# Performance work log

Measured on AMD Instinct MI355X. Metric: run time of the kernel, lower is better.

Reference implementation:

```python
import jax, jax.numpy as jnp
import numpy as np

B, C_IN, N = 2048, 128, 128
M = N - 1  # conv output positions per tree (stride-3 kernel-3 over 3*M gathered triples)


def setup_inputs() -> dict:
    key = jax.random.key(0)
    ks = jax.random.split(key, 8)
    trees = jax.random.normal(ks[0], (B, C_IN, N), jnp.float32)
    trees = trees.at[:, :, 0].set(0.0)  # slot 0 is the zero-pad node
    indexes = jax.random.randint(ks[1], (B, 3 * M), 0, N)

    def wconv(k, o, c):
        return jax.random.normal(k, (o, c, 3), jnp.float32) * 0.05

    return {
        "trees": trees,
        "indexes": indexes,
        "W1": wconv(ks[2], 256, C_IN), "b1": jnp.zeros((256,), jnp.float32),
        "W2": wconv(ks[3], 128, 256), "b2": jnp.zeros((128,), jnp.float32),
        "W3": wconv(ks[4], 64, 128), "b3": jnp.zeros((64,), jnp.float32),
        "W4": jax.random.normal(ks[5], (32, 64), jnp.float32) * 0.1,
        "b4": jnp.zeros((32,), jnp.float32),
        "W5": jax.random.normal(ks[6], (1, 32), jnp.float32) * 0.1,
        "b5": jnp.zeros((1,), jnp.float32),
    }


def _tree_conv(data, idx, W, b):
    # data: [B, C, N]; idx: [B, 3M] of (self, left, right) node indices
    g = jnp.take_along_axis(data, idx[:, None, :], axis=2)        # [B, C, 3M] gather
    g = g.reshape(data.shape[0], data.shape[1], -1, 3)            # [B, C, M, 3]
    out = jnp.einsum('bcmk,ock->bom', g, W) + b[None, :, None]    # Conv1d(k=3, s=3)
    zero = jnp.zeros((out.shape[0], out.shape[1], 1), out.dtype)  # re-prepend zero slot
    return jnp.concatenate([zero, out], axis=2)                   # [B, O, N]


def _tree_layer_norm(data):
    # normalize over (channels, nodes) per tree; torch.std is unbiased (ddof=1)
    mean = jnp.mean(data, axis=(1, 2), keepdims=True)
    std = jnp.std(data, axis=(1, 2), keepdims=True, ddof=1)
    return (data - mean) / (std + 1e-5)


def _leaky(x):
    return jax.nn.leaky_relu(x, 0.01)


def reference(trees, W1, b1, W2, b2, W3, b3, W4, b4, W5, b5, indexes):
    x = _leaky(_tree_layer_norm(_tree_conv(trees, indexes, W1, b1)))
    x = _leaky(_tree_layer_norm(_tree_conv(x, indexes, W2, b2)))
    x = _tree_layer_norm(_tree_conv(x, indexes, W3, b3))
    pooled = jnp.max(x, axis=2)                                   # DynamicPooling -> [B, 64]
    h = _leaky(pooled @ W4.T + b4)
    return h @ W5.T + b5                                          # [B, 1]
```

## Files before the change

kernel.cpp:

```cpp
#include <hip/hip_runtime.h>

typedef unsigned short u16;
typedef __attribute__((ext_vector_type(8)))  short          short8;
typedef __attribute__((ext_vector_type(8)))  unsigned short ushort8v;
typedef __attribute__((ext_vector_type(4)))  unsigned short ushort4v;
typedef __attribute__((ext_vector_type(16))) float          float16v;

__device__ __forceinline__ float bf2f(u16 u){
  union { unsigned int i; float f; } x; x.i = ((unsigned int)u) << 16; return x.f;
}
__device__ __forceinline__ u16 f2bf(float f){
  union { float f; unsigned int i; } x; x.f = f;
  unsigned int u = x.i;
  unsigned int r = (u + 0x7FFFu + ((u >> 16) & 1u)) >> 16;
  return (u16)r;
}
__device__ __forceinline__ float lk(float v){ return v > 0.f ? v : 0.01f*v; }

__global__ void permute_w(const float* __restrict__ W1, const float* __restrict__ W2,
                          const float* __restrict__ W3, u16* __restrict__ ws){
  int t = blockIdx.x*256 + threadIdx.x;
  const float* src; u16* dst; int C, local;
  if (t < 98304)       { src = W1; dst = ws;          C = 128; local = t; }
  else if (t < 196608) { src = W2; dst = ws + 98304;  C = 256; local = t - 98304; }
  else if (t < 221184) { src = W3; dst = ws + 196608; C = 128; local = t - 196608; }
  else return;
  const int NJK  = 3*C/16;
  const int tile = local >> 9, within = local & 511;
  const int lane = within >> 3, e = within & 7;
  const int rb = tile / NJK, jk = tile - rb*NJK;
  const int o  = rb*32 + (lane & 31);
  const int kg = jk*16 + (lane >> 5)*8 + e;
  const int j  = kg / C, c = kg - j*C;
  dst[local] = f2bf(src[o*3*C + c*3 + j]);
}

template<int CIN, int O, int SIN, int OST, int NTL, int NACT, bool LEAKY, bool IS_L3>
__device__ __forceinline__ void do_layer(const u16* __restrict__ Wt,
                                         const float* __restrict__ bias,
                                         const u16* bIn, u16* bOut, float* bOutF,
                                         const int* sidx, float* sstat,
                                         int tid, float* out_mean, float* out_inv)
{
  constexpr int KS  = CIN/16;
  constexpr int NJK = 3*KS;
  static_assert((O/64)*4 == NACT*NTL, "work split mismatch");
  const int w = tid >> 6, lane = tid & 63, l31 = lane & 31, h = lane >> 5;
  const bool active = (w < NACT);
  const int wa = active ? w : 0;

  const int u0  = wa*NTL;
  const int rb  = u0 >> 2;
  const int nt0 = u0 & 3;
  const int r0  = rb * 64;

  const u16* aP[2] = { Wt + ((size_t)(rb*2    )*NJK)*512 + lane*8,
                       Wt + ((size_t)(rb*2 + 1)*NJK)*512 + lane*8 };

  float16v acc[NTL][2];
  float s = 0.f, s2 = 0.f;

  if (active){
    int boff[NTL][3];
#pragma unroll
    for (int n = 0; n < NTL; ++n){
      int m = (nt0 + n)*32 + l31;
#pragma unroll
      for (int j = 0; j < 3; ++j){
        int i = sidx[3*m + j];
        boff[n][j] = i*SIN + h*8;
      }
    }

#pragma unroll
    for (int n = 0; n < NTL; ++n){ acc[n][0] = {}; acc[n][1] = {}; }

#pragma unroll
    for (int jk = 0; jk < NJK; ++jk){
      const int j    = jk / KS;
      const int coff = (jk - j*KS)*16;
      short8 A0 = *(const short8*)(aP[0] + jk*512);
      short8 A1 = *(const short8*)(aP[1] + jk*512);
#pragma unroll
      for (int n = 0; n < NTL; ++n){
        short8 Bf = *(const short8*)(bIn + boff[n][j] + coff);
        acc[n][0] = __builtin_amdgcn_mfma_f32_32x32x16_bf16(A0, Bf, acc[n][0], 0, 0, 0);
        acc[n][1] = __builtin_amdgcn_mfma_f32_32x32x16_bf16(A1, Bf, acc[n][1], 0, 0, 0);
      }
    }

#pragma unroll
    for (int n = 0; n < NTL; ++n){
      const int m = (nt0 + n)*32 + l31;
      const bool valid = (m <= 126);
#pragma unroll
      for (int a = 0; a < 2; ++a)
#pragma unroll
        for (int g = 0; g < 4; ++g){
          const int rowb = r0 + a*32 + 8*g + 4*h;
#pragma unroll
          for (int q = 0; q < 4; ++q){
            float raw = acc[n][a][4*g + q] + bias[rowb + q];
            acc[n][a][4*g + q] = raw;
            if (valid){ s += raw; s2 += raw*raw; }
          }
        }
    }
  }

#pragma unroll
  for (int off = 32; off >= 1; off >>= 1){
    s  += __shfl_down(s,  off, 64);
    s2 += __shfl_down(s2, off, 64);
  }
  if (lane == 0){ sstat[w*2] = s; sstat[w*2+1] = s2; }
  __syncthreads();

  float tot = 0.f, tot2 = 0.f;
#pragma unroll
  for (int q = 0; q < 8; ++q){ tot += sstat[2*q]; tot2 += sstat[2*q+1]; }
  constexpr float CNT = (float)(O * 128);
  const float mean = tot / CNT;
  float var = (tot2 - tot*mean) / (CNT - 1.f);
  var = fmaxf(var, 0.f);
  const float inv = 1.f / (sqrtf(var) + 1e-5f);
  *out_mean = mean; *out_inv = inv;

  if constexpr (!IS_L3){
    if (active){
#pragma unroll
      for (int n = 0; n < NTL; ++n){
        const int m = (nt0 + n)*32 + l31;
        const bool valid = (m <= 126);
#pragma unroll
        for (int a = 0; a < 2; ++a){
#pragma unroll
          for (int g = 0; g < 4; ++g){
            const int rowb = r0 + a*32 + 8*g + 4*h;
            ushort4v pk;
#pragma unroll
            for (int q = 0; q < 4; ++q){
              float f = (acc[n][a][4*g + q] - mean) * inv;
              if constexpr (LEAKY) f = lk(f);
              pk[q] = f2bf(f);
            }
            if (valid) *(ushort4v*)(bOut + (size_t)(m+1)*OST + rowb) = pk;
          }
        }
      }
    }
    if (tid < O/8){
      float f0 = (0.f - mean) * inv;
      if constexpr (LEAKY) f0 = lk(f0);
      const u16 v0 = f2bf(f0);
      ushort8v z;
#pragma unroll
      for (int e = 0; e < 8; ++e) z[e] = v0;
      *(ushort8v*)(bOut + tid*8) = z;
    }
  } else {
    if (active){
#pragma unroll
      for (int n = 0; n < NTL; ++n){
        const int m = (nt0 + n)*32 + l31;
        if (m <= 126){
#pragma unroll
          for (int a = 0; a < 2; ++a)
#pragma unroll
            for (int g = 0; g < 4; ++g){
              const int rowb = r0 + a*32 + 8*g + 4*h;
#pragma unroll
              for (int q = 0; q < 4; ++q)
                bOutF[(size_t)(m+1)*OST + rowb + q] = acc[n][a][4*g + q];
            }
        }
      }
    }
  }
  __syncthreads();
}

__global__ __launch_bounds__(512, 4) void bao_main(
    const float* __restrict__ trees, const int* __restrict__ gidx,
    const u16* __restrict__ wsW,
    const float* __restrict__ b1, const float* __restrict__ b2, const float* __restrict__ b3,
    const float* __restrict__ W4, const float* __restrict__ b4,
    const float* __restrict__ W5, const float* __restrict__ b5,
    float* __restrict__ dout)
{
  __shared__ __align__(16) u16 buf[33792];
  __shared__ int   sidx[384];
  __shared__ float sstat[16];
  __shared__ float spoolP[512];
  __shared__ float spool[64];
  __shared__ float sh[32];

  const int tid = threadIdx.x;
  const int b = blockIdx.x;
  float* bufF = (float*)buf;

  const float* tb = trees + (size_t)b * (128*128);
  {
    const int ngrp = tid & 31, cg = tid >> 5;
    const int c0 = cg*8;
#pragma unroll
    for (int it = 0; it < 4; ++it){
      const int n = ngrp + 32*it;
      ushort8v pk;
#pragma unroll
      for (int cc = 0; cc < 8; ++cc) pk[cc] = f2bf(tb[(c0 + cc)*128 + n]);
      *(ushort8v*)(buf + n*136 + c0) = pk;
    }
  }
  if (tid < 96){
#pragma unroll
    for (int k = 0; k < 4; ++k){
      int ii = tid*4 + k;
      sidx[ii] = (ii < 381) ? gidx[(size_t)b*381 + ii] : 0;
    }
  }
  __syncthreads();

  float mean, inv;
  do_layer<128,256,136,264, 2, 8, true ,false>(wsW,          b1, buf, buf, nullptr, sidx, sstat, tid, &mean, &inv);
  do_layer<256,128,264,136, 1, 8, true ,false>(wsW + 98304,  b2, buf, buf, nullptr, sidx, sstat, tid, &mean, &inv);
  do_layer<128, 64,136, 67, 1, 4, false,true >(wsW + 196608, b3, buf, nullptr, bufF, sidx, sstat, tid, &mean, &inv);

  {
    const int ch = tid & 63, seg = tid >> 6;
    float mx = 0.f;
    const int nd0 = seg*16 + (seg == 0 ? 1 : 0);
    for (int nd = nd0; nd < seg*16 + 16; ++nd) mx = fmaxf(mx, bufF[nd*67 + ch]);
    spoolP[seg*64 + ch] = mx;
  }
  __syncthreads();
  if (tid < 64){
    float mx = spoolP[tid];
#pragma unroll
    for (int k = 1; k < 8; ++k) mx = fmaxf(mx, spoolP[64*k + tid]);
    spool[tid] = (mx - mean) * inv;
  }
  __syncthreads();
  if (tid < 32){
    float a = b4[tid];
    for (int c = 0; c < 64; ++c) a += spool[c] * W4[tid*64 + c];
    sh[tid] = lk(a);
  }
  __syncthreads();
  if (tid == 0){
    float o = b5[0];
    for (int i = 0; i < 32; ++i) o += sh[i] * W5[i];
    dout[b] = o;
  }
}

extern "C" void kernel_launch(void* const* d_in, const int* in_sizes, int n_in,
                              void* d_out, int out_size, void* d_ws, size_t ws_size,
                              hipStream_t stream) {
  const float* trees = (const float*)d_in[0];
  const int*   gidx  = (const int*)d_in[1];
  const float* W1 = (const float*)d_in[2];
  const float* b1 = (const float*)d_in[3];
  const float* W2 = (const float*)d_in[4];
  const float* b2 = (const float*)d_in[5];
  const float* W3 = (const float*)d_in[6];
  const float* b3 = (const float*)d_in[7];
  const float* W4 = (const float*)d_in[8];
  const float* b4 = (const float*)d_in[9];
  const float* W5 = (const float*)d_in[10];
  const float* b5 = (const float*)d_in[11];
  u16* wsW = (u16*)d_ws;

  permute_w<<<864, 256, 0, stream>>>(W1, W2, W3, wsW);
  bao_main<<<2048, 512, 0, stream>>>(trees, gidx, wsW, b1, b2, b3, W4, b4, W5, b5,
                                     (float*)d_out);
}
```

Measured before the change: 346.4 us.

## Process two trees per block to reuse weight fragments across trees

Each block now handles two trees. Every weight A-fragment loaded from global memory feeds MFMAs for both trees, which halves weight traffic per tree. Accumulator registers double and LDS per block doubles to about 140KB, so launch bounds drop to 2 blocks per CU and the grid halves to 1024 blocks. The cost is lower occupancy and less latency hiding, plus possible register pressure.

```diff
diff --git a/kernel.cpp b/kernel.cpp
--- a/kernel.cpp
+++ b/kernel.cpp
@@ -36,11 +36,14 @@
 }
 
 template<int CIN, int O, int SIN, int OST, int NTL, int NACT, bool LEAKY, bool IS_L3>
-__device__ __forceinline__ void do_layer(const u16* __restrict__ Wt,
-                                         const float* __restrict__ bias,
-                                         const u16* bIn, u16* bOut, float* bOutF,
-                                         const int* sidx, float* sstat,
-                                         int tid, float* out_mean, float* out_inv)
+__device__ __forceinline__ void do_layer2(const u16* __restrict__ Wt,
+                                          const float* __restrict__ bias,
+                                          const u16* bIn0, const u16* bIn1,
+                                          u16* bOut0, u16* bOut1,
+                                          float* bOutF0, float* bOutF1,
+                                          const int* sidx0, const int* sidx1,
+                                          float* sstat, int tid,
+                                          float* mean2, float* inv2)
 {
   constexpr int KS  = CIN/16;
   constexpr int NJK = 3*KS;
@@ -54,125 +57,154 @@
   const int nt0 = u0 & 3;
   const int r0  = rb * 64;
 
-  const u16* aP[2] = { Wt + ((size_t)(rb*2    )*NJK)*512 + lane*8,
-                       Wt + ((size_t)(rb*2 + 1)*NJK)*512 + lane*8 };
-
-  float16v acc[NTL][2];
-  float s = 0.f, s2 = 0.f;
+  const u16* aP0 = Wt + ((size_t)(rb*2    )*NJK)*512 + lane*8;
+  const u16* aP1 = Wt + ((size_t)(rb*2 + 1)*NJK)*512 + lane*8;
+
+  float16v acc[2][NTL][2];
+  float s[2] = {0.f, 0.f}, s2[2] = {0.f, 0.f};
 
   if (active){
-    int boff[NTL][3];
+    int boff[2][NTL][3];
 #pragma unroll
     for (int n = 0; n < NTL; ++n){
       int m = (nt0 + n)*32 + l31;
 #pragma unroll
       for (int j = 0; j < 3; ++j){
-        int i = sidx[3*m + j];
-        boff[n][j] = i*SIN + h*8;
-      }
-    }
-
-#pragma unroll
-    for (int n = 0; n < NTL; ++n){ acc[n][0] = {}; acc[n][1] = {}; }
+        boff[0][n][j] = sidx0[3*m + j]*SIN + h*8;
+        boff[1][n][j] = sidx1[3*m + j]*SIN + h*8;
+      }
+    }
+
+#pragma unroll
+    for (int t = 0; t < 2; ++t)
+#pragma unroll
+      for (int n = 0; n < NTL; ++n){ acc[t][n][0] = {}; acc[t][n][1] = {}; }
 
 #pragma unroll
     for (int jk = 0; jk < NJK; ++jk){
       const int j    = jk / KS;
       const int coff = (jk - j*KS)*16;
-      short8 A0 = *(const short8*)(aP[0] + jk*512);
-      short8 A1 = *(const short8*)(aP[1] + jk*512);
-#pragma unroll
-      for (int n = 0; n < NTL; ++n){
-        short8 Bf = *(const short8*)(bIn + boff[n][j] + coff);
-        acc[n][0] = __builtin_amdgcn_mfma_f32_32x32x16_bf16(A0, Bf, acc[n][0], 0, 0, 0);
-        acc[n][1] = __builtin_amdgcn_mfma_f32_32x32x16_bf16(A1, Bf, acc[n][1], 0, 0, 0);
-      }
-    }
-
-#pragma unroll
-    for (int n = 0; n < NTL; ++n){
-      const int m = (nt0 + n)*32 + l31;
-      const bool valid = (m <= 126);
-#pragma unroll
-      for (int a = 0; a < 2; ++a)
-#pragma unroll
-        for (int g = 0; g < 4; ++g){
-          const int rowb = r0 + a*32 + 8*g + 4*h;
-#pragma unroll
-          for (int q = 0; q < 4; ++q){
-            float raw = acc[n][a][4*g + q] + bias[rowb + q];
-            acc[n][a][4*g + q] = raw;
-            if (valid){ s += raw; s2 += raw*raw; }
-          }
+      short8 A0 = *(const short8*)(aP0 + jk*512);
+      short8 A1 = *(const short8*)(aP1 + jk*512);
+#pragma unroll
+      for (int t = 0; t < 2; ++t){
+        const u16* bb = t ? bIn1 : bIn0;
+#pragma unroll
+        for (int n = 0; n < NTL; ++n){
+          short8 Bf = *(const short8*)(bb + boff[t][n][j] + coff);
+          acc[t][n][0] = __builtin_amdgcn_mfma_f32_32x32x16_bf16(A0, Bf, acc[t][n][0], 0, 0, 0);
+          acc[t][n][1] = __builtin_amdgcn_mfma_f32_32x32x16_bf16(A1, Bf, acc[t][n][1], 0, 0, 0);
         }
-    }
-  }
-
-#pragma unroll
-  for (int off = 32; off >= 1; off >>= 1){
-    s  += __shfl_down(s,  off, 64);
-    s2 += __shfl_down(s2, off, 64);
-  }
-  if (lane == 0){ sstat[w*2] = s; sstat[w*2+1] = s2; }
-  __syncthreads();
-
-  float tot = 0.f, tot2 = 0.f;
-#pragma unroll
-  for (int q = 0; q < 8; ++q){ tot += sstat[2*q]; tot2 += sstat[2*q+1]; }
-  constexpr float CNT = (float)(O * 128);
-  const float mean = tot / CNT;
-  float var = (tot2 - tot*mean) / (CNT - 1.f);
-  var = fmaxf(var, 0.f);
-  const float inv = 1.f / (sqrtf(var) + 1e-5f);
-  *out_mean = mean; *out_inv = inv;
-
-  if constexpr (!IS_L3){
-    if (active){
+      }
+    }
+
+#pragma unroll
+    for (int t = 0; t < 2; ++t)
 #pragma unroll
       for (int n = 0; n < NTL; ++n){
         const int m = (nt0 + n)*32 + l31;
         const bool valid = (m <= 126);
 #pragma unroll
-        for (int a = 0; a < 2; ++a){
+        for (int a = 0; a < 2; ++a)
 #pragma unroll
           for (int g = 0; g < 4; ++g){
             const int rowb = r0 + a*32 + 8*g + 4*h;
-            ushort4v pk;
 #pragma unroll
             for (int q = 0; q < 4; ++q){
-              float f = (acc[n][a][4*g + q] - mean) * inv;
-              if constexpr (LEAKY) f = lk(f);
-              pk[q] = f2bf(f);
+              float raw = acc[t][n][a][4*g + q] + bias[rowb + q];
+              acc[t][n][a][4*g + q] = raw;
+              if (valid){ s[t] += raw; s2[t] += raw*raw; }
             }
-            if (valid) *(ushort4v*)(bOut + (size_t)(m+1)*OST + rowb) = pk;
+          }
+      }
+  }
+
+#pragma unroll
+  for (int off = 32; off >= 1; off >>= 1){
+#pragma unroll
+    for (int t = 0; t < 2; ++t){
+      s[t]  += __shfl_down(s[t],  off, 64);
+      s2[t] += __shfl_down(s2[t], off, 64);
+    }
+  }
+  if (lane == 0){
+    sstat[w*4 + 0] = s[0];  sstat[w*4 + 1] = s2[0];
+    sstat[w*4 + 2] = s[1];  sstat[w*4 + 3] = s2[1];
+  }
+  __syncthreads();
+
+#pragma unroll
+  for (int t = 0; t < 2; ++t){
+    float tot = 0.f, tot2 = 0.f;
+#pragma unroll
+    for (int q = 0; q < 8; ++q){ tot += sstat[q*4 + t*2]; tot2 += sstat[q*4 + t*2 + 1]; }
+    constexpr float CNT = (float)(O * 128);
+    const float mean = tot / CNT;
+    float var = (tot2 - tot*mean) / (CNT - 1.f);
+    var = fmaxf(var, 0.f);
+    const float inv = 1.f / (sqrtf(var) + 1e-5f);
+    mean2[t] = mean; inv2[t] = inv;
+  }
+
+  if constexpr (!IS_L3){
+    if (active){
+#pragma unroll
+      for (int t = 0; t < 2; ++t){
+        u16* bo = t ? bOut1 : bOut0;
+        const float mean = mean2[t], inv = inv2[t];
+#pragma unroll
+        for (int n = 0; n < NTL; ++n){
+          const int m = (nt0 + n)*32 + l31;
+          const bool valid = (m <= 126);
+#pragma unroll
+          for (int a = 0; a < 2; ++a){
+#pragma unroll
+            for (int g = 0; g < 4; ++g){
+              const int rowb = r0 + a*32 + 8*g + 4*h;
+              ushort4v pk;
+#pragma unroll
+              for (int q = 0; q < 4; ++q){
+                float f = (acc[t][n][a][4*g + q] - mean) * inv;
+                if constexpr (LEAKY) f = lk(f);
+                pk[q] = f2bf(f);
+              }
+              if (valid) *(ushort4v*)(bo + (size_t)(m+1)*OST + rowb) = pk;
+            }
           }
         }
       }
     }
     if (tid < O/8){
-      float f0 = (0.f - mean) * inv;
-      if constexpr (LEAKY) f0 = lk(f0);
-      const u16 v0 = f2bf(f0);
-      ushort8v z;
-#pragma unroll
-      for (int e = 0; e < 8; ++e) z[e] = v0;
-      *(ushort8v*)(bOut + tid*8) = z;
+#pragma unroll
+      for (int t = 0; t < 2; ++t){
+        float f0 = (0.f - mean2[t]) * inv2[t];
+        if constexpr (LEAKY) f0 = lk(f0);
+        const u16 v0 = f2bf(f0);
+        ushort8v z;
+#pragma unroll
+        for (int e = 0; e < 8; ++e) z[e] = v0;
+        *(ushort8v*)((t ? bOut1 : bOut0) + tid*8) = z;
+      }
     }
   } else {
     if (active){
 #pragma unroll
-      for (int n = 0; n < NTL; ++n){
-        const int m = (nt0 + n)*32 + l31;
-        if (m <= 126){
-#pragma unroll
-          for (int a = 0; a < 2; ++a)
-#pragma unroll
-            for (int g = 0; g < 4; ++g){
-              const int rowb = r0 + a*32 + 8*g + 4*h;
-#pragma unroll
-              for (int q = 0; q < 4; ++q)
-                bOutF[(size_t)(m+1)*OST + rowb + q] = acc[n][a][4*g + q];
-            }
+      for (int t = 0; t < 2; ++t){
+        float* bo = t ? bOutF1 : bOutF0;
+#pragma unroll
+        for (int n = 0; n < NTL; ++n){
+          const int m = (nt0 + n)*32 + l31;
+          if (m <= 126){
+#pragma unroll
+            for (int a = 0; a < 2; ++a)
+#pragma unroll
+              for (int g = 0; g < 4; ++g){
+                const int rowb = r0 + a*32 + 8*g + 4*h;
+#pragma unroll
+                for (int q = 0; q < 4; ++q)
+                  bo[(size_t)(m+1)*OST + rowb + q] = acc[t][n][a][4*g + q];
+              }
+          }
         }
       }
     }
@@ -180,7 +212,7 @@
   __syncthreads();
 }
 
-__global__ __launch_bounds__(512, 4) void bao_main(
+__global__ __launch_bounds__(512, 2) void bao_main(
     const float* __restrict__ trees, const int* __restrict__ gidx,
     const u16* __restrict__ wsW,
     const float* __restrict__ b1, const float* __restrict__ b2, const float* __restrict__ b3,
@@ -188,69 +220,83 @@
     const float* __restrict__ W5, const float* __restrict__ b5,
     float* __restrict__ dout)
 {
-  __shared__ __align__(16) u16 buf[33792];
-  __shared__ int   sidx[384];
-  __shared__ float sstat[16];
-  __shared__ float spoolP[512];
-  __shared__ float spool[64];
-  __shared__ float sh[32];
+  __shared__ __align__(16) u16 buf0[33792];
+  __shared__ __align__(16) u16 buf1[33792];
+  __shared__ int   sidx[2][384];
+  __shared__ float sstat[32];
+  __shared__ float spoolP[2][256];
+  __shared__ float spool[2][64];
+  __shared__ float sh[2][32];
 
   const int tid = threadIdx.x;
-  const int b = blockIdx.x;
-  float* bufF = (float*)buf;
-
-  const float* tb = trees + (size_t)b * (128*128);
+  const int b0 = blockIdx.x * 2;
+  float* bufF0 = (float*)buf0;
+  float* bufF1 = (float*)buf1;
+
   {
-    const int ngrp = tid & 31, cg = tid >> 5;
-    const int c0 = cg*8;
-#pragma unroll
-    for (int it = 0; it < 4; ++it){
-      const int n = ngrp + 32*it;
+    const int half = tid >> 8, t2 = tid & 255;
+    const float* tb = trees + (size_t)(b0 + half) * (128*128);
+    u16* bufS = half ? buf1 : buf0;
+    const int ngrp = t2 & 31, cg = t2 >> 5;
+#pragma unroll
+    for (int it = 0; it < 8; ++it){
+      const int n  = ngrp + 32*(it & 3);
+      const int c0 = (cg + 8*(it >> 2))*8;
       ushort8v pk;
 #pragma unroll
       for (int cc = 0; cc < 8; ++cc) pk[cc] = f2bf(tb[(c0 + cc)*128 + n]);
-      *(ushort8v*)(buf + n*136 + c0) = pk;
-    }
-  }
-  if (tid < 96){
+      *(ushort8v*)(bufS + n*136 + c0) = pk;
+    }
+  }
+  if (tid < 192){
+    const int tr = tid / 96, bt = tid - tr*96;
 #pragma unroll
     for (int k = 0; k < 4; ++k){
-      int ii = tid*4 + k;
-      sidx[ii] = (ii < 381) ? gidx[(size_t)b*381 + ii] : 0;
-    }
-  }
-  __syncthreads();
-
-  float mean, inv;
-  do_layer<128,256,136,264, 2, 8, true ,false>(wsW,          b1, buf, buf, nullptr, sidx, sstat, tid, &mean, &inv);
-  do_layer<256,128,264,136, 1, 8, true ,false>(wsW + 98304,  b2, buf, buf, nullptr, sidx, sstat, tid, &mean, &inv);
-  do_layer<128, 64,136, 67, 1, 4, false,true >(wsW + 196608, b3, buf, nullptr, bufF, sidx, sstat, tid, &mean, &inv);
+      int ii = bt*4 + k;
+      sidx[tr][ii] = (ii < 381) ? gidx[(size_t)(b0 + tr)*381 + ii] : 0;
+    }
+  }
+  __syncthreads();
+
+  float mean2[2], inv2[2];
+  do_layer2<128,256,136,264, 2, 8, true ,false>(wsW,          b1, buf0, buf1, buf0, buf1,
+                                                nullptr, nullptr, sidx[0], sidx[1],
+                                                sstat, tid, mean2, inv2);
+  do_layer2<256,128,264,136, 1, 8, true ,false>(wsW + 98304,  b2, buf0, buf1, buf0, buf1,
+                                                nullptr, nullptr, sidx[0], sidx[1],
+                                                sstat, tid, mean2, inv2);
+  do_layer2<128, 64,136, 67, 1, 4, false,true >(wsW + 196608, b3, buf0, buf1, nullptr, nullptr,
+                                                bufF0, bufF1, sidx[0], sidx[1],
+                                                sstat, tid, mean2, inv2);
 
   {
-    const int ch = tid & 63, seg = tid >> 6;
+    const int tr = tid >> 8, t2 = tid & 255;
+    const int ch = t2 & 63, seg = t2 >> 6;
+    const float* bF = tr ? bufF1 : bufF0;
     float mx = 0.f;
-    const int nd0 = seg*16 + (seg == 0 ? 1 : 0);
-    for (int nd = nd0; nd < seg*16 + 16; ++nd) mx = fmaxf(mx, bufF[nd*67 + ch]);
-    spoolP[seg*64 + ch] = mx;
+    const int nd0 = seg*32 + (seg == 0 ? 1 : 0);
+    for (int nd = nd0; nd < seg*32 + 32; ++nd) mx = fmaxf(mx, bF[nd*67 + ch]);
+    spoolP[tr][seg*64 + ch] = mx;
+  }
+  __syncthreads();
+  if (tid < 128){
+    const int tr = tid >> 6, ch = tid & 63;
+    float mx = fmaxf(fmaxf(spoolP[tr][ch], spoolP[tr][64 + ch]),
+                     fmaxf(spoolP[tr][128 + ch], spoolP[tr][192 + ch]));
+    spool[tr][ch] = (mx - mean2[tr]) * inv2[tr];
   }
   __syncthreads();
   if (tid < 64){
-    float mx = spoolP[tid];
-#pragma unroll
-    for (int k = 1; k < 8; ++k) mx = fmaxf(mx, spoolP[64*k + tid]);
-    spool[tid] = (mx - mean) * inv;
-  }
-  __syncthreads();
-  if (tid < 32){
-    float a = b4[tid];
-    for (int c = 0; c < 64; ++c) a += spool[c] * W4[tid*64 + c];
-    sh[tid] = lk(a);
-  }
-  __syncthreads();
-  if (tid == 0){
+    const int tr = tid >> 5, r = tid & 31;
+    float a = b4[r];
+    for (int c = 0; c < 64; ++c) a += spool[tr][c] * W4[r*64 + c];
+    sh[tr][r] = lk(a);
+  }
+  __syncthreads();
+  if (tid < 2){
     float o = b5[0];
-    for (int i = 0; i < 32; ++i) o += sh[i] * W5[i];
-    dout[b] = o;
+    for (int i = 0; i < 32; ++i) o += sh[tid][i] * W5[i];
+    dout[b0 + tid] = o;
   }
 }
 
@@ -272,6 +318,6 @@
   u16* wsW = (u16*)d_ws;
 
   permute_w<<<864, 256, 0, stream>>>(W1, W2, W3, wsW);
-  bao_main<<<2048, 512, 0, stream>>>(trees, gidx, wsW, b1, b2, b3, W4, b4, W5, b5,
+  bao_main<<<1024, 512, 0, stream>>>(trees, gidx, wsW, b1, b2, b3, W4, b4, W5, b5,
                                      (float*)d_out);
 }
```

New measurement: 363.0 us. +4.8%, slower.
